# Performance work log

Measured on AMD Instinct MI355X. Metric: run time of the kernel, lower is better.

## Reference

```python
import jax, jax.numpy as jnp
import numpy as np

K = 3      # kernel_size
S = 2      # stride
EPS = 1e-5 # BatchNorm eps


def setup_inputs() -> dict:
    key = jax.random.key(0)
    ks = jax.random.split(key, 6)
    B, C, H, W = 8, 256, 128, 128
    k2 = K * K
    return {
        "x": jax.random.normal(ks[0], (B, C, H, W), jnp.float32),
        "w_conv": jax.random.normal(ks[1], (k2, C, K, K), jnp.float32) * 0.05,
        "bn_gamma": jnp.ones((k2,), jnp.float32),
        "bn_beta": jnp.zeros((k2,), jnp.float32),
        "bn_mean": jax.random.normal(ks[2], (k2,), jnp.float32) * 0.1,
        "bn_var": jnp.ones((k2,), jnp.float32),
        "ch_w1": jax.random.normal(ks[3], (C // 4, C), jnp.float32) * 0.05,
        "ch_w2": jax.random.normal(ks[4], (C, C // 4), jnp.float32) * 0.05,
    }


def reference(x, w_conv, bn_gamma, bn_beta, bn_mean, bn_var, ch_w1, ch_w2):
    b, c, h, w = x.shape
    oh = (h - 1) // S + 1
    ow = (w - 1) // S + 1
    # weight_net: strided KxK conv (C -> k2) + eval-mode BatchNorm
    wlog = jax.lax.conv_general_dilated(
        x, w_conv, window_strides=(S, S), padding=((1, 1), (1, 1)),
        dimension_numbers=("NCHW", "OIHW", "NCHW"))  # (b, k2, oh, ow)
    scale = bn_gamma / jnp.sqrt(bn_var + EPS)
    wlog = (wlog - bn_mean[None, :, None, None]) * scale[None, :, None, None] \
        + bn_beta[None, :, None, None]
    # channel_net: GAP -> 1x1 conv -> relu -> 1x1 conv (all bias-free)
    gap = x.mean(axis=(2, 3))                      # (b, c)
    ch = jax.nn.relu(gap @ ch_w1.T) @ ch_w2.T      # (b, c)
    # per-pixel, per-channel logits over the k^2 taps; softmax over taps
    logits = wlog[:, None] * ch[:, :, None, None, None]  # (b, c, k2, oh, ow)
    attn = jax.nn.softmax(logits, axis=2)
    # unfold: reflect pad then KxK patches with stride S (tap order row-major,
    # matching torch unfold(2,.).unfold(3,.) and the k2->(k,k) reshape)
    px = jnp.pad(x, ((0, 0), (0, 0), (1, 1), (1, 1)), mode="reflect")
    taps = []
    for di in range(K):
        for dj in range(K):
            taps.append(px[:, :, di:di + (oh - 1) * S + 1:S,
                           dj:dj + (ow - 1) * S + 1:S])
    patches = jnp.stack(taps, axis=2)              # (b, c, k2, oh, ow)
    return (attn * patches).sum(axis=2)            # (b, c, oh, ow)
```

## Files before the change

### kernel.cpp

```cpp
#include <hip/hip_runtime.h>
#include <hip/hip_bf16.h>


#define EPS 1e-5f
#define CH_SPLIT 4
#define CH_PER_WAVE 16

__global__ __launch_bounds__(256) void prep_kernel(
    const float* __restrict__ wconv, const float* __restrict__ gamma,
    const float* __restrict__ beta, const float* __restrict__ mean,
    const float* __restrict__ var, float* __restrict__ wt,
    float* __restrict__ bias, float* __restrict__ gap) {
  const int c = threadIdx.x;
  #pragma unroll
  for (int t = 0; t < 9; ++t) {
    float sc = gamma[t] * rsqrtf(var[t] + EPS);
    #pragma unroll
    for (int p = 0; p < 9; ++p)
      wt[c * 84 + t * 9 + p] = wconv[((size_t)t * 256 + c) * 9 + p] * sc;
  }
  wt[c * 84 + 81] = 0.f;
  wt[c * 84 + 82] = 0.f;
  wt[c * 84 + 83] = 0.f;
  if (c < 9) bias[c] = beta[c] - mean[c] * gamma[c] * rsqrtf(var[c] + EPS);
  else if (c < 16) bias[c] = 0.f;
  #pragma unroll
  for (int k = 0; k < 8; ++k) gap[k * 256 + c] = 0.f;
}

__global__ __launch_bounds__(256) void init_wlog_kernel(
    const float* __restrict__ bias, float* __restrict__ wlog) {
  const int idx = blockIdx.x * 256 + threadIdx.x;
  const int t = idx % 12;
  wlog[idx] = (t < 9) ? bias[t] : 0.f;
}

__global__ __launch_bounds__(256, 2) void conv_kernel(
    const float* __restrict__ x, const float* __restrict__ wt,
    float* __restrict__ wlog, float* __restrict__ gap) {
  const int j = threadIdx.x & 63;
  const int wv = threadIdx.x >> 6;
  const int i0 = blockIdx.x * 4;
  const int b = blockIdx.y;
  const int z = blockIdx.z;
  const int cbase = __builtin_amdgcn_readfirstlane((z * 4 + wv) * CH_PER_WAVE);

  float acc[4][9];
  #pragma unroll
  for (int ri = 0; ri < 4; ++ri)
    #pragma unroll
    for (int t = 0; t < 9; ++t) acc[ri][t] = 0.f;

  const float* xb = x + ((size_t)b * 256 + cbase) * 16384;
  const float4* wq = (const float4*)(wt + (size_t)cbase * 84);
  const int h0 = 2 * i0 - 1;

  for (int c = 0; c < CH_PER_WAVE; ++c, xb += 16384, wq += 21) {
    float2 v[9];
    #pragma unroll
    for (int r = 0; r < 9; ++r) {
      const int hh = h0 + r;
      if ((unsigned)hh < 128u)
        v[r] = *(const float2*)(xb + hh * 128 + 2 * j);
      else
        v[r] = make_float2(0.f, 0.f);
    }
    float lf[9];
    #pragma unroll
    for (int r = 0; r < 9; ++r) {
      float t = __shfl_up(v[r].y, 1, 64);
      lf[r] = (j == 0) ? 0.f : t;
    }
    float gs = 0.f;
    #pragma unroll
    for (int r = 1; r < 9; ++r) gs += v[r].x + v[r].y;
    #pragma unroll
    for (int off = 32; off; off >>= 1) gs += __shfl_xor(gs, off, 64);
    if (j == 0) atomicAdd(&gap[b * 256 + cbase + c], gs);

    float4 w4[21];
    #pragma unroll
    for (int q = 0; q < 21; ++q) w4[q] = wq[q];
    const float* w = (const float*)w4;

    #pragma unroll
    for (int ri = 0; ri < 4; ++ri) {
      #pragma unroll
      for (int ki = 0; ki < 3; ++ki) {
        const int r = 2 * ri + ki;
        const float x0 = lf[r], x1 = v[r].x, x2 = v[r].y;
        #pragma unroll
        for (int t = 0; t < 9; ++t) {
          float a = acc[ri][t];
          a = fmaf(x0, w[t * 9 + ki * 3 + 0], a);
          a = fmaf(x1, w[t * 9 + ki * 3 + 1], a);
          a = fmaf(x2, w[t * 9 + ki * 3 + 2], a);
          acc[ri][t] = a;
        }
      }
    }
  }

  __shared__ float red[4][64][9];
  #pragma unroll
  for (int ri = 0; ri < 4; ++ri) {
    __syncthreads();
    #pragma unroll
    for (int t = 0; t < 9; ++t) red[wv][j][t] = acc[ri][t];
    __syncthreads();
    const size_t rowpos = ((size_t)b * 64 + (i0 + ri)) * 64;
    for (int idx = threadIdx.x; idx < 576; idx += 256) {
      const int jj = idx / 9, tt = idx - jj * 9;
      float s =
          red[0][jj][tt] + red[1][jj][tt] + red[2][jj][tt] + red[3][jj][tt];
      atomicAdd(&wlog[(rowpos + jj) * 12 + tt], s);
    }
  }
}

__global__ __launch_bounds__(256) void chnet_kernel(
    const float* __restrict__ gap, const float* __restrict__ w1,
    const float* __restrict__ w2, float* __restrict__ ch) {
  const int b = blockIdx.x;
  __shared__ float g[256];
  __shared__ float h[64];
  const int t = threadIdx.x;
  g[t] = gap[b * 256 + t] * (1.f / 16384.f);
  __syncthreads();
  if (t < 64) {
    float s = 0.f;
    const float* w = w1 + t * 256;
    for (int c = 0; c < 256; ++c) s += g[c] * w[c];
    h[t] = fmaxf(s, 0.f);
  }
  __syncthreads();
  float s = 0.f;
  const float* w = w2 + t * 64;
  #pragma unroll 4
  for (int j = 0; j < 64; ++j) s += h[j] * w[j];
  ch[b * 256 + t] = s;
}

__global__ __launch_bounds__(256) void final_kernel(
    const float* __restrict__ x, const float* __restrict__ wlog,
    const float* __restrict__ ch, float* __restrict__ out) {
  const int j = threadIdx.x & 63;
  const int il = threadIdx.x >> 6;
  const int i = blockIdx.x * 4 + il;
  const int c = blockIdx.y;
  const int b = blockIdx.z;
  const float chv = ch[b * 256 + c];

  const size_t pos = ((size_t)b * 64 + i) * 64 + j;
  const float4* wp = (const float4*)(wlog + pos * 12);
  float4 wa = wp[0], wb = wp[1], wcv = wp[2];
  float lg[9] = {wa.x, wa.y, wa.z, wa.w, wb.x, wb.y, wb.z, wb.w, wcv.x};

  float m = -3.4e38f;
  #pragma unroll
  for (int t = 0; t < 9; ++t) {
    lg[t] *= chv;
    m = fmaxf(m, lg[t]);
  }
  float e[9], s = 0.f;
  #pragma unroll
  for (int t = 0; t < 9; ++t) {
    e[t] = __expf(lg[t] - m);
    s += e[t];
  }
  const float inv = 1.f / s;

  const float* xp = x + ((size_t)b * 256 + c) * 16384;
  float acc = 0.f;
  #pragma unroll
  for (int ki = 0; ki < 3; ++ki) {
    int hh = 2 * i - 1 + ki;
    hh = hh < 0 ? -hh : hh;
    float2 v = *(const float2*)(xp + hh * 128 + 2 * j);
    float left = __shfl_up(v.y, 1, 64);
    acc += e[ki * 3 + 0] * left + e[ki * 3 + 1] * v.x + e[ki * 3 + 2] * v.y;
  }
  out[(size_t)(b * 256 + c) * 4096 + i * 64 + j] = acc * inv;
}

extern "C" void kernel_launch(void* const* d_in, const int* in_sizes, int n_in,
                              void* d_out, int out_size, void* d_ws,
                              size_t ws_size, hipStream_t stream) {
  const float* x = (const float*)d_in[0];
  const float* w_conv = (const float*)d_in[1];
  const float* bn_gamma = (const float*)d_in[2];
  const float* bn_beta = (const float*)d_in[3];
  const float* bn_mean = (const float*)d_in[4];
  const float* bn_var = (const float*)d_in[5];
  const float* ch_w1 = (const float*)d_in[6];
  const float* ch_w2 = (const float*)d_in[7];
  float* out = (float*)d_out;

  float* wsf = (float*)d_ws;
  float* gap = wsf;
  float* ch = wsf + 2048;
  float* bias = wsf + 4096;
  float* wt = wsf + 4112;
  float* wlog = wsf + 25616;

  prep_kernel<<<1, 256, 0, stream>>>(w_conv, bn_gamma, bn_beta, bn_mean,
                                     bn_var, wt, bias, gap);
  init_wlog_kernel<<<1536, 256, 0, stream>>>(bias, wlog);
  conv_kernel<<<dim3(16, 8, CH_SPLIT), 256, 0, stream>>>(x, wt, wlog, gap);
  chnet_kernel<<<8, 256, 0, stream>>>(gap, ch_w1, ch_w2, ch);
  final_kernel<<<dim3(16, 256, 8), 256, 0, stream>>>(x, wlog, ch, out);
}
```

Before: 94.25 us.

## Fuse prep kernels, split conv channels further, loop channels in final kernel

Merges the weight-prep and wlog-init kernels into one launch, so the bias is now computed per block. The conv kernel gets a finer channel split (8 instead of 4, with 8 channels per wave) and a higher occupancy bound. Its weights are re-laid out by kernel row so each row loads only 7 float4s, which cuts register pressure. The final kernel now loops over 32 channels per block, reusing the wlog load, and launches far fewer blocks, which in turn reduces parallelism for that stage.

```diff
diff --git a/kernel.cpp b/kernel.cpp
--- a/kernel.cpp
+++ b/kernel.cpp
@@ -3,39 +3,43 @@
 
 
 #define EPS 1e-5f
-#define CH_SPLIT 4
-#define CH_PER_WAVE 16
-
-__global__ __launch_bounds__(256) void prep_kernel(
+#define CH_SPLIT 8
+#define CH_PER_WAVE 8
+
+__global__ __launch_bounds__(256) void prep_init_kernel(
     const float* __restrict__ wconv, const float* __restrict__ gamma,
     const float* __restrict__ beta, const float* __restrict__ mean,
     const float* __restrict__ var, float* __restrict__ wt,
-    float* __restrict__ bias, float* __restrict__ gap) {
-  const int c = threadIdx.x;
-  #pragma unroll
-  for (int t = 0; t < 9; ++t) {
-    float sc = gamma[t] * rsqrtf(var[t] + EPS);
-    #pragma unroll
-    for (int p = 0; p < 9; ++p)
-      wt[c * 84 + t * 9 + p] = wconv[((size_t)t * 256 + c) * 9 + p] * sc;
-  }
-  wt[c * 84 + 81] = 0.f;
-  wt[c * 84 + 82] = 0.f;
-  wt[c * 84 + 83] = 0.f;
-  if (c < 9) bias[c] = beta[c] - mean[c] * gamma[c] * rsqrtf(var[c] + EPS);
-  else if (c < 16) bias[c] = 0.f;
-  #pragma unroll
-  for (int k = 0; k < 8; ++k) gap[k * 256 + c] = 0.f;
-}
-
-__global__ __launch_bounds__(256) void init_wlog_kernel(
-    const float* __restrict__ bias, float* __restrict__ wlog) {
-  const int idx = blockIdx.x * 256 + threadIdx.x;
-  const int t = idx % 12;
-  wlog[idx] = (t < 9) ? bias[t] : 0.f;
-}
-
-__global__ __launch_bounds__(256, 2) void conv_kernel(
+    float* __restrict__ gap, float* __restrict__ wlog) {
+  const int blk = blockIdx.x;
+  if (blk < 1536) {
+    float biasv[9];
+    #pragma unroll
+    for (int t = 0; t < 9; ++t)
+      biasv[t] = beta[t] - mean[t] * gamma[t] * rsqrtf(var[t] + EPS);
+    const int idx = blk * 256 + threadIdx.x;
+    const int t = idx % 12;
+    wlog[idx] = (t < 9) ? biasv[t] : 0.f;
+  } else {
+    const int c = threadIdx.x;
+    #pragma unroll
+    for (int t = 0; t < 9; ++t) {
+      float sc = gamma[t] * rsqrtf(var[t] + EPS);
+      #pragma unroll
+      for (int ki = 0; ki < 3; ++ki)
+        #pragma unroll
+        for (int kj = 0; kj < 3; ++kj)
+          wt[c * 84 + ki * 28 + t * 3 + kj] =
+              wconv[((size_t)t * 256 + c) * 9 + ki * 3 + kj] * sc;
+    }
+    #pragma unroll
+    for (int ki = 0; ki < 3; ++ki) wt[c * 84 + ki * 28 + 27] = 0.f;
+    #pragma unroll
+    for (int k = 0; k < 8; ++k) gap[k * 256 + c] = 0.f;
+  }
+}
+
+__global__ __launch_bounds__(256, 4) void conv_kernel(
     const float* __restrict__ x, const float* __restrict__ wt,
     float* __restrict__ wlog, float* __restrict__ gap) {
   const int j = threadIdx.x & 63;
@@ -52,10 +56,10 @@
     for (int t = 0; t < 9; ++t) acc[ri][t] = 0.f;
 
   const float* xb = x + ((size_t)b * 256 + cbase) * 16384;
-  const float4* wq = (const float4*)(wt + (size_t)cbase * 84);
+  const float* wcb = wt + (size_t)cbase * 84;
   const int h0 = 2 * i0 - 1;
 
-  for (int c = 0; c < CH_PER_WAVE; ++c, xb += 16384, wq += 21) {
+  for (int c = 0; c < CH_PER_WAVE; ++c, xb += 16384, wcb += 84) {
     float2 v[9];
     #pragma unroll
     for (int r = 0; r < 9; ++r) {
@@ -78,23 +82,23 @@
     for (int off = 32; off; off >>= 1) gs += __shfl_xor(gs, off, 64);
     if (j == 0) atomicAdd(&gap[b * 256 + cbase + c], gs);
 
-    float4 w4[21];
-    #pragma unroll
-    for (int q = 0; q < 21; ++q) w4[q] = wq[q];
-    const float* w = (const float*)w4;
-
-    #pragma unroll
-    for (int ri = 0; ri < 4; ++ri) {
+    #pragma unroll
+    for (int ki = 0; ki < 3; ++ki) {
+      float4 wk[7];
+      const float4* wq = (const float4*)(wcb + ki * 28);
       #pragma unroll
-      for (int ki = 0; ki < 3; ++ki) {
+      for (int q = 0; q < 7; ++q) wk[q] = wq[q];
+      const float* w = (const float*)wk;
+      #pragma unroll
+      for (int ri = 0; ri < 4; ++ri) {
         const int r = 2 * ri + ki;
         const float x0 = lf[r], x1 = v[r].x, x2 = v[r].y;
         #pragma unroll
         for (int t = 0; t < 9; ++t) {
           float a = acc[ri][t];
-          a = fmaf(x0, w[t * 9 + ki * 3 + 0], a);
-          a = fmaf(x1, w[t * 9 + ki * 3 + 1], a);
-          a = fmaf(x2, w[t * 9 + ki * 3 + 2], a);
+          a = fmaf(x0, w[t * 3 + 0], a);
+          a = fmaf(x1, w[t * 3 + 1], a);
+          a = fmaf(x2, w[t * 3 + 2], a);
           acc[ri][t] = a;
         }
       }
@@ -147,40 +151,54 @@
   const int j = threadIdx.x & 63;
   const int il = threadIdx.x >> 6;
   const int i = blockIdx.x * 4 + il;
-  const int c = blockIdx.y;
-  const int b = blockIdx.z;
-  const float chv = ch[b * 256 + c];
+  const int b = blockIdx.y;
+  const int c0 = blockIdx.z * 32;
 
   const size_t pos = ((size_t)b * 64 + i) * 64 + j;
   const float4* wp = (const float4*)(wlog + pos * 12);
   float4 wa = wp[0], wb = wp[1], wcv = wp[2];
-  float lg[9] = {wa.x, wa.y, wa.z, wa.w, wb.x, wb.y, wb.z, wb.w, wcv.x};
-
-  float m = -3.4e38f;
-  #pragma unroll
-  for (int t = 0; t < 9; ++t) {
-    lg[t] *= chv;
-    m = fmaxf(m, lg[t]);
-  }
-  float e[9], s = 0.f;
-  #pragma unroll
-  for (int t = 0; t < 9; ++t) {
-    e[t] = __expf(lg[t] - m);
-    s += e[t];
-  }
-  const float inv = 1.f / s;
-
-  const float* xp = x + ((size_t)b * 256 + c) * 16384;
-  float acc = 0.f;
-  #pragma unroll
-  for (int ki = 0; ki < 3; ++ki) {
-    int hh = 2 * i - 1 + ki;
-    hh = hh < 0 ? -hh : hh;
-    float2 v = *(const float2*)(xp + hh * 128 + 2 * j);
-    float left = __shfl_up(v.y, 1, 64);
-    acc += e[ki * 3 + 0] * left + e[ki * 3 + 1] * v.x + e[ki * 3 + 2] * v.y;
-  }
-  out[(size_t)(b * 256 + c) * 4096 + i * 64 + j] = acc * inv;
+  const float wl[9] = {wa.x, wa.y, wa.z, wa.w, wb.x, wb.y, wb.z, wb.w, wcv.x};
+
+  const float* chp = ch + b * 256 + c0;
+  const float* xp0 = x + ((size_t)b * 256 + c0) * 16384;
+  float* op = out + ((size_t)b * 256 + c0) * 4096 + i * 64 + j;
+
+  for (int c = 0; c < 32; ++c) {
+    const float chv = chp[c];
+    const float* xp = xp0 + (size_t)c * 16384;
+
+    float2 v0, v1, v2;
+    {
+      int hh = 2 * i - 1;
+      hh = hh < 0 ? -hh : hh;
+      v0 = *(const float2*)(xp + hh * 128 + 2 * j);
+      v1 = *(const float2*)(xp + (2 * i) * 128 + 2 * j);
+      v2 = *(const float2*)(xp + (2 * i + 1) * 128 + 2 * j);
+    }
+
+    float lg[9], m = -3.4e38f;
+    #pragma unroll
+    for (int t = 0; t < 9; ++t) {
+      lg[t] = wl[t] * chv;
+      m = fmaxf(m, lg[t]);
+    }
+    float e[9], s = 0.f;
+    #pragma unroll
+    for (int t = 0; t < 9; ++t) {
+      e[t] = __expf(lg[t] - m);
+      s += e[t];
+    }
+    const float inv = 1.f / s;
+
+    float l0 = __shfl_up(v0.y, 1, 64);
+    float l1 = __shfl_up(v1.y, 1, 64);
+    float l2 = __shfl_up(v2.y, 1, 64);
+    float acc = e[0] * l0 + e[1] * v0.x + e[2] * v0.y;
+    acc += e[3] * l1 + e[4] * v1.x + e[5] * v1.y;
+    acc += e[6] * l2 + e[7] * v2.x + e[8] * v2.y;
+
+    op[(size_t)c * 4096] = acc * inv;
+  }
 }
 
 extern "C" void kernel_launch(void* const* d_in, const int* in_sizes, int n_in,
@@ -199,14 +217,12 @@
   float* wsf = (float*)d_ws;
   float* gap = wsf;
   float* ch = wsf + 2048;
-  float* bias = wsf + 4096;
-  float* wt = wsf + 4112;
-  float* wlog = wsf + 25616;
-
-  prep_kernel<<<1, 256, 0, stream>>>(w_conv, bn_gamma, bn_beta, bn_mean,
-                                     bn_var, wt, bias, gap);
-  init_wlog_kernel<<<1536, 256, 0, stream>>>(bias, wlog);
+  float* wt = wsf + 4096;
+  float* wlog = wsf + 25600;
+
+  prep_init_kernel<<<1537, 256, 0, stream>>>(w_conv, bn_gamma, bn_beta,
+                                             bn_mean, bn_var, wt, gap, wlog);
   conv_kernel<<<dim3(16, 8, CH_SPLIT), 256, 0, stream>>>(x, wt, wlog, gap);
   chnet_kernel<<<8, 256, 0, stream>>>(gap, ch_w1, ch_w2, ch);
-  final_kernel<<<dim3(16, 256, 8), 256, 0, stream>>>(x, wlog, ch, out);
-}
+  final_kernel<<<dim3(16, 8, 8), 256, 0, stream>>>(x, wlog, ch, out);
+}
```

Measured after the change: 86.11 us. 1.09x faster.
